# Kernel tuning notes

Measured on AMD Instinct MI355X. Metric: run time of the kernel, lower is better.

Reference implementation:

```python
import jax, jax.numpy as jnp
import numpy as np

N_IN = 2_000_000
N_OUT = 250_000
C_IN = 32
C_OUT = 64
K_VOL = 8  # 2x2x2 kernel, stride 2
EPS = 1e-5


def setup_inputs() -> dict:
    key = jax.random.key(0)
    ks = jax.random.split(key, 6)
    return {
        "in_feats": jax.random.normal(ks[0], (N_IN, C_IN), dtype=jnp.float32),
        "offset_id": jax.random.randint(ks[1], (N_IN,), 0, K_VOL, dtype=jnp.int32),
        "out_idx": jax.random.randint(ks[2], (N_IN,), 0, N_OUT, dtype=jnp.int32),
        "weight": jax.random.normal(ks[3], (K_VOL, C_IN, C_OUT), dtype=jnp.float32) * 0.05,
        "gamma": jnp.ones((3, C_OUT), dtype=jnp.float32),
        "beta": jnp.zeros((3, C_OUT), dtype=jnp.float32),
        "context": jax.random.normal(ks[4], (256,), dtype=jnp.float32),
        "ctx_w": jax.random.normal(ks[5], (256, 2 * C_OUT), dtype=jnp.float32) * 0.02,
        "condition": 1,
    }


def reference(in_feats, offset_id, out_idx, weight, gamma, beta, context, ctx_w, condition):
    # --- sparse conv (stride == kernel): gather-GEMM-scatter per kernel tap ---
    out = jnp.zeros((N_OUT, C_OUT), dtype=in_feats.dtype)
    for k in range(K_VOL):  # fixed small loop over kernel taps
        xk = jnp.where((offset_id == k)[:, None], in_feats, 0.0)  # [N_in, C_in]
        contrib = xk @ weight[k]                                  # [N_in, C_out]
        out = out + jax.ops.segment_sum(contrib, out_idx, num_segments=N_OUT)
    # --- conditional BN (PDNorm-style): per-channel stats, condition-selected affine ---
    mean = jnp.mean(out, axis=0)
    var = jnp.var(out, axis=0)
    normed = (out - mean) * jax.lax.rsqrt(var + EPS)
    normed = normed * gamma[condition] + beta[condition]
    # context modulation: scale/shift from context vector
    scale, shift = jnp.split(context @ ctx_w, 2)  # each [C_out]
    normed = normed * (1.0 + scale) + shift
    # --- ReLU ---
    return jax.nn.relu(normed)
```

## Files before the change

### kernel.cpp

```cpp
#include <hip/hip_runtime.h>

#define N_IN 2000000
#define N_OUT 250000
#define C_IN 32
#define C_OUT 64
#define K_VOL 8
#define EPS 1e-5f
#define CAP 32

#define PT_BLOCKS 7813
#define N_SCAN 250112
#define N_SBLK 977

typedef __attribute__((ext_vector_type(8))) short short8;
typedef __attribute__((ext_vector_type(4))) float f32x4;

#define TA_WHL    250368
#define TA_BSUM   266752
#define TA_SMALL  267776
#define TA_CNT    268288
#define TA_IDXG   1018400
#define TA_POS    (TA_IDXG + N_IN)
#define TA_NEED_BYTES ((size_t)(TA_POS + N_IN) * 4)

#define T1_WT     250000
#define T1_SMALL  266384
#define T1_RLIST  266768
#define T1_NEED_BYTES ((size_t)(T1_RLIST + N_OUT * CAP) * 4)

__global__ __launch_bounds__(256) void k_rank(const int* __restrict__ out_idx,
                                              int* __restrict__ cnt,
                                              int* __restrict__ pos0,
                                              float* __restrict__ smalls) {
    int b = blockIdx.x;
    if (b < PT_BLOCKS) {
        int i = b * 256 + threadIdx.x;
        if (i < N_IN) pos0[i] = atomicAdd(&cnt[out_idx[i]], 1);
    } else {
        if (threadIdx.x < 128) smalls[threadIdx.x] = 0.f;
    }
}

__global__ __launch_bounds__(256) void k_scan_a(const int* __restrict__ cnt,
                                                int* __restrict__ S,
                                                int* __restrict__ bsum) {
    __shared__ int sh[256];
    int t = threadIdx.x;
    int g = blockIdx.x * 256 + t;
    int v = cnt[g];
    sh[t] = v;
    __syncthreads();
#pragma unroll
    for (int off = 1; off < 256; off <<= 1) {
        int a = (t >= off) ? sh[t - off] : 0;
        __syncthreads();
        sh[t] += a;
        __syncthreads();
    }
    S[g] = sh[t] - v;
    if (t == 255) bsum[blockIdx.x] = sh[255];
}

__global__ __launch_bounds__(256) void k_scan_c2(int* __restrict__ S,
                                                 const int* __restrict__ bsum) {
    __shared__ int red[256];
    int t = threadIdx.x, bid = blockIdx.x;
    int acc = 0;
    for (int j = t; j < bid; j += 256) acc += bsum[j];
    red[t] = acc;
    __syncthreads();
#pragma unroll
    for (int off = 128; off > 0; off >>= 1) {
        if (t < off) red[t] += red[t + off];
        __syncthreads();
    }
    S[bid * 256 + t] += red[0];
}

__global__ __launch_bounds__(256) void k_scatidx(const int* __restrict__ out_idx,
                                                 const int* __restrict__ offs,
                                                 const int* __restrict__ pos0,
                                                 const int* __restrict__ S,
                                                 const float* __restrict__ w,
                                                 int* __restrict__ idxg,
                                                 ushort* __restrict__ whl) {
    int b = blockIdx.x;
    if (b < PT_BLOCKS) {
        int i = b * 256 + threadIdx.x;
        if (i >= N_IN) return;
        int o = out_idx[i];
        int tag = offs[i] | ((o & 31) << 3);
        idxg[S[o] + pos0[i]] = i | (tag << 21);
    } else {
        int e = (b - PT_BLOCKS) * 256 + threadIdx.x;
        int c = e >> 11, t = (e >> 9) & 3, l = (e >> 3) & 63, kp = e & 7;
        int j = 4 * c + (l >> 4);
        int n = t * 16 + (l & 15);
        float v = w[kp * 2048 + j * 64 + n];
        unsigned bits = __float_as_uint(v);
        float lo = v - __uint_as_float(bits & 0xFFFF0000u);
        whl[e]         = (ushort)(bits >> 16);
        whl[16384 + e] = (ushort)(__float_as_uint(lo) >> 16);
    }
}

__global__ __launch_bounds__(256) void k_gconv12(const float* __restrict__ xf,
                                                 const int* __restrict__ idxg,
                                                 const int* __restrict__ Sarr,
                                                 const ushort* __restrict__ whl,
                                                 float* __restrict__ out) {
    __shared__ float vxl[4 * 3104];
    int lane = threadIdx.x & 63;
    int wv = threadIdx.x >> 6;
    int g = blockIdx.x * 4 + wv;
    int base = g * 8;
    if (base >= N_OUT) return;
    float* VX = vxl + wv * 3104;
    short* XT = (short*)VX;

    int s = Sarr[base];
    int e = Sarr[base + 8];
    int slot = lane >> 3, jq = lane & 7;

    int tgt4[4];
#pragma unroll
    for (int m = 0; m < 4; ++m) {
        int bin0 = m * 16 + (lane & 15);
        tgt4[m] = (((base + (bin0 >> 3)) & 31) << 3) | (bin0 & 7);
    }

    f32x4 acc1[4][2];
#pragma unroll
    for (int m = 0; m < 4; ++m)
#pragma unroll
        for (int n = 0; n < 2; ++n)
            acc1[m][n] = (f32x4){0.f, 0.f, 0.f, 0.f};

    auto LOADBLK = [&](int p0, float4* xvv, int* tvv) {
        int pk[4];
#pragma unroll
        for (int q = 0; q < 4; ++q) {
            int p = p0 + q * 8 + slot;
            int pc = p < e ? p : e - 1;
            pk[q] = idxg[pc];
        }
#pragma unroll
        for (int q = 0; q < 4; ++q) {
            int p = p0 + q * 8 + slot;
            int idx = pk[q] & 0x1FFFFF;
            tvv[q] = (pk[q] >> 21) & 0xFF;
            xvv[q] = *(const float4*)(xf + (size_t)idx * 32 + jq * 4);
            if (p >= e) xvv[q] = make_float4(0.f, 0.f, 0.f, 0.f);
        }
    };
    auto STAGE = [&](int bb, const float4* xvv, const int* tvv) {
        short* Xh = XT + bb * 3104;
        short* Xl = Xh + 1536;
        unsigned char* TGb = (unsigned char*)(Xh + 3072);
#pragma unroll
        for (int q = 0; q < 4; ++q) {
            int wpos = ((q ^ (jq & 3)) << 3) + slot;
#pragma unroll
            for (int i = 0; i < 4; ++i) {
                float v = (i == 0) ? xvv[q].x : (i == 1) ? xvv[q].y
                         : (i == 2) ? xvv[q].z : xvv[q].w;
                unsigned b = __float_as_uint(v);
                float lo = v - __uint_as_float(b & 0xFFFF0000u);
                int ch = 4 * jq + i;
                Xh[ch * 48 + wpos] = (short)(b >> 16);
                Xl[ch * 48 + wpos] = (short)(__float_as_uint(lo) >> 16);
            }
            if (jq == 0) TGb[q * 8 + slot] = (unsigned char)tvv[q];
        }
    };

    if (e > s) {
        float4 xvA[4], xvB[4], xvC[4];
        int tvA[4], tvB[4], tvC[4];
        int nIt = (e - s + 31) >> 5;
        LOADBLK(s, xvA, tvA);
        LOADBLK(s + 32, xvB, tvB);
        STAGE(0, xvA, tvA);
        for (int it = 0; it < nIt; ++it) {
            int cur = it & 1;
            if (it + 2 < nIt) LOADBLK(s + (it + 2) * 32, xvC, tvC);

            asm volatile("s_waitcnt lgkmcnt(0)" ::: "memory");

            const short* Xh = XT + cur * 3104;
            const short* Xl = Xh + 1536;
            const unsigned char* TGb = (const unsigned char*)(Xh + 3072);
            unsigned long long t8 = *(const unsigned long long*)(TGb + 8 * (lane >> 4));
            int tgv[8];
#pragma unroll
            for (int e2 = 0; e2 < 8; ++e2) tgv[e2] = (int)((t8 >> (8 * e2)) & 0xFF);
            short8 bhf[2], blf[2];
#pragma unroll
            for (int n = 0; n < 2; ++n) {
                int ch = n * 16 + (lane & 15);
                int off = ch * 48 + 8 * ((lane >> 4) ^ ((ch >> 2) & 3));
                bhf[n] = *(const short8*)(Xh + off);
                blf[n] = *(const short8*)(Xl + off);
            }

            if (it + 1 < nIt) STAGE(cur ^ 1, xvB, tvB);
            __builtin_amdgcn_sched_barrier(0);

#pragma unroll
            for (int m = 0; m < 4; ++m) {
                short8 ah;
#pragma unroll
                for (int e2 = 0; e2 < 8; ++e2)
                    ah[e2] = (tgv[e2] == tgt4[m]) ? (short)0x3F80 : (short)0;
#pragma unroll
                for (int n = 0; n < 2; ++n) {
                    acc1[m][n] = __builtin_amdgcn_mfma_f32_16x16x32_bf16(ah, bhf[n], acc1[m][n], 0, 0, 0);
                    acc1[m][n] = __builtin_amdgcn_mfma_f32_16x16x32_bf16(ah, blf[n], acc1[m][n], 0, 0, 0);
                }
            }

            if (it + 1 < nIt) {
#pragma unroll
                for (int q = 0; q < 4; ++q) { xvB[q] = xvC[q]; tvB[q] = tvC[q]; }
            }
        }
    }

    asm volatile("s_waitcnt lgkmcnt(0)" ::: "memory");

#pragma unroll
    for (int m = 0; m < 4; ++m)
#pragma unroll
        for (int n = 0; n < 2; ++n)
#pragma unroll
            for (int reg = 0; reg < 4; ++reg) {
                int bin = m * 16 + (lane >> 4) * 4 + reg;
                VX[(bin >> 3) * 289 + (n * 16 + (lane & 15)) * 9 + (bin & 7)] = acc1[m][n][reg];
            }

    __builtin_amdgcn_sched_barrier(0);
    asm volatile("s_waitcnt lgkmcnt(0)" ::: "memory");
    __builtin_amdgcn_sched_barrier(0);

    int o = lane >> 4;
    int n16 = lane & 15;
    f32x4 zacc = {0.f, 0.f, 0.f, 0.f};
    f32x4 acc0 = zacc, accA = zacc, accB = zacc, accC = zacc;
    const short8* wh = (const short8*)whl;
    const short8* wl = wh + 2048;

#pragma unroll
    for (int c = 0; c < 8; ++c) {
        float a[8];
        if (n16 < 8) {
            const float* src = VX + n16 * 289 + (4 * c + o) * 9;
#pragma unroll
            for (int el = 0; el < 8; ++el) a[el] = src[el];
        } else {
#pragma unroll
            for (int el = 0; el < 8; ++el) a[el] = 0.f;
        }
        short8 ahi, alo;
#pragma unroll
        for (int el = 0; el < 8; ++el) {
            unsigned b = __float_as_uint(a[el]);
            ahi[el] = (short)(b >> 16);
            float lo = a[el] - __uint_as_float(b & 0xFFFF0000u);
            alo[el] = (short)(__float_as_uint(lo) >> 16);
        }
#pragma unroll
        for (int t = 0; t < 4; ++t) {
            short8 bh = wh[(c * 4 + t) * 64 + lane];
            short8 bl = wl[(c * 4 + t) * 64 + lane];
            f32x4* pa = (t == 0) ? &acc0 : (t == 1) ? &accA : (t == 2) ? &accB : &accC;
            *pa = __builtin_amdgcn_mfma_f32_16x16x32_bf16(ahi, bh, *pa, 0, 0, 0);
            *pa = __builtin_amdgcn_mfma_f32_16x16x32_bf16(alo, bh, *pa, 0, 0, 0);
            *pa = __builtin_amdgcn_mfma_f32_16x16x32_bf16(ahi, bl, *pa, 0, 0, 0);
        }
    }

    if (o < 2) {
#pragma unroll
        for (int t = 0; t < 4; ++t) {
            f32x4 a = (t == 0) ? acc0 : (t == 1) ? accA : (t == 2) ? accB : accC;
#pragma unroll
            for (int reg = 0; reg < 4; ++reg)
                out[(size_t)(base + o * 4 + reg) * 64 + t * 16 + n16] = a[reg];
        }
    }
}


__global__ __launch_bounds__(256) void k_stats(const float* __restrict__ out,
                                               float* __restrict__ sums,
                                               float* __restrict__ sumsq) {
    int t = threadIdx.x;
    long stride = (long)gridDim.x * 256;
    float s = 0.f, q = 0.f;
    for (long i = (long)blockIdx.x * 256 + t; i < (long)N_OUT * C_OUT; i += stride) {
        float v = out[i];
        s += v;
        q = fmaf(v, v, q);
    }
    __shared__ float ls[256], lq[256];
    ls[t] = s; lq[t] = q;
    __syncthreads();
    if (t < 64) {
        s = ls[t] + ls[t + 64] + ls[t + 128] + ls[t + 192];
        q = lq[t] + lq[t + 64] + lq[t + 128] + lq[t + 192];
        atomicAdd(&sums[t], s);
        atomicAdd(&sumsq[t], q);
    }
}

__global__ __launch_bounds__(256) void k_ctxprep(const float* __restrict__ context,
                                                 const float* __restrict__ ctx_w,
                                                 const float* __restrict__ sums,
                                                 const float* __restrict__ sumsq,
                                                 const float* __restrict__ gamma,
                                                 const float* __restrict__ beta,
                                                 const int* __restrict__ cond,
                                                 float* __restrict__ AB) {
    __shared__ float part[256];
    __shared__ float ctxv[128];
    int t = threadIdx.x;
    int col = t & 127, half = t >> 7;
    float s = 0.f;
    for (int r = half * 128; r < half * 128 + 128; ++r)
        s = fmaf(context[r], ctx_w[r * 128 + col], s);
    part[t] = s;
    __syncthreads();
    if (t < 128) ctxv[t] = part[t] + part[t + 128];
    __syncthreads();
    if (t < 64) {
        float mean = sums[t] * (1.f / N_OUT);
        float var  = sumsq[t] * (1.f / N_OUT) - mean * mean;
        float inv  = rsqrtf(var + EPS);
        int cd = cond[0];
        float gm = gamma[cd * C_OUT + t], bt = beta[cd * C_OUT + t];
        float sc = 1.f + ctxv[t];
        float sh = ctxv[64 + t];
        AB[t]      = inv * gm * sc;
        AB[64 + t] = (bt - mean * inv * gm) * sc + sh;
    }
}

__global__ __launch_bounds__(256) void k_norm(float* __restrict__ out,
                                              const float* __restrict__ AB) {
    __shared__ float4 lA[16], lB[16];
    int t = threadIdx.x;
    if (t < 16) {
        lA[t] = ((const float4*)AB)[t];
        lB[t] = ((const float4*)AB)[16 + t];
    }
    __syncthreads();
    const long total4 = (long)N_OUT * C_OUT / 4;
    long stride = (long)gridDim.x * 256;
    for (long i = (long)blockIdx.x * 256 + t; i < total4; i += stride) {
        float4 v = ((float4*)out)[i];
        float4 a = lA[i & 15], b = lB[i & 15];
        v.x = fmaxf(fmaf(v.x, a.x, b.x), 0.f);
        v.y = fmaxf(fmaf(v.y, a.y, b.y), 0.f);
        v.z = fmaxf(fmaf(v.z, a.z, b.z), 0.f);
        v.w = fmaxf(fmaf(v.w, a.w, b.w), 0.f);
        ((float4*)out)[i] = v;
    }
}


__global__ __launch_bounds__(256) void k_scat2(const int* __restrict__ out_idx,
                                               const int* __restrict__ offs,
                                               const float* __restrict__ w,
                                               int* __restrict__ cnt,
                                               int* __restrict__ rlist,
                                               ushort* __restrict__ whl) {
    int b = blockIdx.x;
    if (b < PT_BLOCKS) {
        int i = b * 256 + threadIdx.x;
        if (i < N_IN) {
            int o = out_idx[i];
            int pos = atomicAdd(&cnt[o], 1);
            if (pos < CAP) rlist[o * CAP + pos] = i | (offs[i] << 21);
        }
    } else {
        int e = (b - PT_BLOCKS) * 256 + threadIdx.x;
        int c = e >> 11, t = (e >> 9) & 3, l = (e >> 3) & 63, kp = e & 7;
        int j = 4 * c + (l >> 4);
        int n = t * 16 + (l & 15);
        float v = w[kp * 2048 + j * 64 + n];
        unsigned bits = __float_as_uint(v);
        float lo = v - __uint_as_float(bits & 0xFFFF0000u);
        whl[e]         = (ushort)(bits >> 16);
        whl[16384 + e] = (ushort)(__float_as_uint(lo) >> 16);
    }
}

__global__ __launch_bounds__(128) void k_gconv3(const float* __restrict__ xf,
                                                const int* __restrict__ cnt,
                                                const int* __restrict__ rlist,
                                                const ushort* __restrict__ whl,
                                                float* __restrict__ out) {
    __shared__ float vxl[2 * 4640];
    int lane = threadIdx.x & 63;
    int wv = threadIdx.x >> 6;
    int g = blockIdx.x * 2 + wv;
    int base = g * 16;
    if (base >= N_OUT) return;
    float* VX = vxl + wv * 4640;

    float4* z4 = (float4*)VX;
    float4 zz = make_float4(0.f, 0.f, 0.f, 0.f);
#pragma unroll
    for (int i = 0; i < 19; ++i) {
        int p = i * 64 + lane;
        if (p < 1156) z4[p] = zz;
    }

    int slot = lane >> 3, jq = lane & 7;
    int cv = cnt[base + (lane & 15)];
    const int* rbase = rlist + (size_t)base * CAP;
    int pkA = rbase[slot * CAP + jq];
    int pkB = rbase[(8 + slot) * CAP + jq];
    int pkC = rbase[slot * CAP + 8 + jq];
    int pkD = rbase[(8 + slot) * CAP + 8 + jq];

#pragma unroll
    for (int r = 0; r < 16; ++r) {
        int cr = __builtin_amdgcn_readlane(cv, r);
        if (cr > CAP) cr = CAP;
        if (cr == 0) continue;
        {
            int pk = __shfl(r < 8 ? pkA : pkB, (r & 7) * 8 + slot, 64);
            int idx = pk & 0x1FFFFF; if (idx > N_IN - 1) idx = N_IN - 1;
            int kp = (pk >> 21) & 7;
            const float4 x = *(const float4*)(xf + (size_t)idx * 32 + jq * 4);
            float* dst = VX + r * 289 + 36 * jq + kp;
            if (slot < cr) {
                atomicAdd(dst + 0,  x.x);
                atomicAdd(dst + 9,  x.y);
                atomicAdd(dst + 18, x.z);
                atomicAdd(dst + 27, x.w);
            }
        }
        if (cr > 8) {
            int pk = __shfl(r < 8 ? pkC : pkD, (r & 7) * 8 + slot, 64);
            int idx = pk & 0x1FFFFF; if (idx > N_IN - 1) idx = N_IN - 1;
            int kp = (pk >> 21) & 7;
            const float4 x = *(const float4*)(xf + (size_t)idx * 32 + jq * 4);
            float* dst = VX + r * 289 + 36 * jq + kp;
            if (8 + slot < cr) {
                atomicAdd(dst + 0,  x.x);
                atomicAdd(dst + 9,  x.y);
                atomicAdd(dst + 18, x.z);
                atomicAdd(dst + 27, x.w);
            }
        }
        if (cr > 16) {
            for (int p0 = 16; p0 < cr; p0 += 8) {
                int pp = p0 + slot; if (pp > cr - 1) pp = cr - 1;
                int pk = rlist[((size_t)base + r) * CAP + pp];
                int idx = pk & 0x1FFFFF; if (idx > N_IN - 1) idx = N_IN - 1;
                int kp = (pk >> 21) & 7;
                const float4 x = *(const float4*)(xf + (size_t)idx * 32 + jq * 4);
                float* dst = VX + r * 289 + 36 * jq + kp;
                if (p0 + slot < cr) {
                    atomicAdd(dst + 0,  x.x);
                    atomicAdd(dst + 9,  x.y);
                    atomicAdd(dst + 18, x.z);
                    atomicAdd(dst + 27, x.w);
                }
            }
        }
    }

    __builtin_amdgcn_sched_barrier(0);
    asm volatile("s_waitcnt lgkmcnt(0)" ::: "memory");
    __builtin_amdgcn_sched_barrier(0);

    int o = lane >> 4;
    int n16 = lane & 15;
    f32x4 zacc = {0.f, 0.f, 0.f, 0.f};
    f32x4 acc0 = zacc, acc1 = zacc, acc2 = zacc, acc3 = zacc;
    const short8* wh = (const short8*)whl;
    const short8* wl = wh + 2048;

#pragma unroll
    for (int c = 0; c < 8; ++c) {
        const float* src = VX + n16 * 289 + (4 * c + o) * 9;
        float a[8];
#pragma unroll
        for (int el = 0; el < 8; ++el) a[el] = src[el];
        short8 ahi, alo;
#pragma unroll
        for (int el = 0; el < 8; ++el) {
            unsigned b = __float_as_uint(a[el]);
            ahi[el] = (short)(b >> 16);
            float lo = a[el] - __uint_as_float(b & 0xFFFF0000u);
            alo[el] = (short)(__float_as_uint(lo) >> 16);
        }
#pragma unroll
        for (int t = 0; t < 4; ++t) {
            short8 bh = wh[(c * 4 + t) * 64 + lane];
            short8 bl = wl[(c * 4 + t) * 64 + lane];
            f32x4* pa = (t == 0) ? &acc0 : (t == 1) ? &acc1 : (t == 2) ? &acc2 : &acc3;
            *pa = __builtin_amdgcn_mfma_f32_16x16x32_bf16(ahi, bh, *pa, 0, 0, 0);
            *pa = __builtin_amdgcn_mfma_f32_16x16x32_bf16(alo, bh, *pa, 0, 0, 0);
            *pa = __builtin_amdgcn_mfma_f32_16x16x32_bf16(ahi, bl, *pa, 0, 0, 0);
        }
    }

#pragma unroll
    for (int t = 0; t < 4; ++t) {
        f32x4 a = (t == 0) ? acc0 : (t == 1) ? acc1 : (t == 2) ? acc2 : acc3;
#pragma unroll
        for (int reg = 0; reg < 4; ++reg)
            out[(size_t)(base + o * 4 + reg) * 64 + t * 16 + n16] = a[reg];
    }
}


extern "C" void kernel_launch(void* const* d_in, const int* in_sizes, int n_in,
                              void* d_out, int out_size, void* d_ws, size_t ws_size,
                              hipStream_t stream) {
    const float* in_feats = (const float*)d_in[0];
    const int*   offs     = (const int*)d_in[1];
    const int*   out_idx  = (const int*)d_in[2];
    const float* weight   = (const float*)d_in[3];
    const float* gamma    = (const float*)d_in[4];
    const float* beta     = (const float*)d_in[5];
    const float* context  = (const float*)d_in[6];
    const float* ctx_w    = (const float*)d_in[7];
    const int*   cond     = (const int*)d_in[8];
    float* out = (float*)d_out;

    int*   wsi = (int*)d_ws;
    float* wsf = (float*)d_ws;

    if (ws_size >= TA_NEED_BYTES) {
        int*    S      = wsi;
        ushort* whl    = (ushort*)(wsf + TA_WHL);
        int*    bsum   = wsi + TA_BSUM;
        float*  smalls = wsf + TA_SMALL;
        int*    cnt    = wsi + TA_CNT;
        int*    idxg   = wsi + TA_IDXG;
        int*    pos0   = wsi + TA_POS;

        hipMemsetAsync(cnt, 0, (size_t)N_SCAN * 4, stream);

        k_rank<<<PT_BLOCKS + 1, 256, 0, stream>>>(out_idx, cnt, pos0, smalls);
        k_scan_a<<<N_SBLK, 256, 0, stream>>>(cnt, S, bsum);
        k_scan_c2<<<N_SBLK, 256, 0, stream>>>(S, bsum);
        k_scatidx<<<PT_BLOCKS + 64, 256, 0, stream>>>(out_idx, offs, pos0, S,
                                                      weight, idxg, whl);
        k_gconv12<<<7813, 256, 0, stream>>>(in_feats, idxg, wsi, whl, out);

        k_stats<<<2048, 256, 0, stream>>>(out, smalls, smalls + 64);
        k_ctxprep<<<1, 256, 0, stream>>>(context, ctx_w, smalls, smalls + 64,
                                         gamma, beta, cond, smalls + 128);
        k_norm<<<2048, 256, 0, stream>>>(out, smalls + 128);
    } else {
        int*    cnt    = wsi;
        ushort* whl    = (ushort*)(wsf + T1_WT);
        float*  smalls = wsf + T1_SMALL;
        int*    rlist  = wsi + T1_RLIST;

        hipMemsetAsync(cnt, 0, (size_t)N_OUT * 4, stream);
        hipMemsetAsync(smalls, 0, 128 * 4, stream);

        k_scat2<<<PT_BLOCKS + 64, 256, 0, stream>>>(out_idx, offs, weight, cnt, rlist, whl);
        k_gconv3<<<7813, 128, 0, stream>>>(in_feats, cnt, rlist, whl, out);

        k_stats<<<2048, 256, 0, stream>>>(out, smalls, smalls + 64);
        k_ctxprep<<<1, 256, 0, stream>>>(context, ctx_w, smalls, smalls + 64,
                                         gamma, beta, cond, smalls + 128);
        k_norm<<<2048, 256, 0, stream>>>(out, smalls + 128);
    }
}
```

Before: 408.2 us.

## Fuse BN statistics into the gather-conv epilogue with per-wave partials

The conv kernel now reduces per-channel sum and sum-of-squares from its MFMA accumulators. Each wave writes its partials to a channel-major workspace buffer, and a small 128-block kernel reduces them. This replaces the separate k_stats pass that re-read the full 64 MB output. The cost is extra shuffles and stores in the conv epilogue, a larger workspace, and reliance on rows outside the valid range contributing zero to the partials.

```diff
diff --git a/kernel.cpp b/kernel.cpp
--- a/kernel.cpp
+++ b/kernel.cpp
@@ -11,6 +11,7 @@
 #define PT_BLOCKS 7813
 #define N_SCAN 250112
 #define N_SBLK 977
+#define NWAVE 31252
 
 typedef __attribute__((ext_vector_type(8))) short short8;
 typedef __attribute__((ext_vector_type(4))) float f32x4;
@@ -21,24 +22,20 @@
 #define TA_CNT    268288
 #define TA_IDXG   1018400
 #define TA_POS    (TA_IDXG + N_IN)
-#define TA_NEED_BYTES ((size_t)(TA_POS + N_IN) * 4)
+#define TA_PART   (TA_POS + N_IN)
+#define TA_NEED_BYTES ((size_t)(TA_PART + 128 * NWAVE) * 4)
 
 #define T1_WT     250000
 #define T1_SMALL  266384
 #define T1_RLIST  266768
 #define T1_NEED_BYTES ((size_t)(T1_RLIST + N_OUT * CAP) * 4)
 
+
 __global__ __launch_bounds__(256) void k_rank(const int* __restrict__ out_idx,
                                               int* __restrict__ cnt,
-                                              int* __restrict__ pos0,
-                                              float* __restrict__ smalls) {
-    int b = blockIdx.x;
-    if (b < PT_BLOCKS) {
-        int i = b * 256 + threadIdx.x;
-        if (i < N_IN) pos0[i] = atomicAdd(&cnt[out_idx[i]], 1);
-    } else {
-        if (threadIdx.x < 128) smalls[threadIdx.x] = 0.f;
-    }
+                                              int* __restrict__ pos0) {
+    int i = blockIdx.x * 256 + threadIdx.x;
+    if (i < N_IN) pos0[i] = atomicAdd(&cnt[out_idx[i]], 1);
 }
 
 __global__ __launch_bounds__(256) void k_scan_a(const int* __restrict__ cnt,
@@ -104,11 +101,12 @@
     }
 }
 
-__global__ __launch_bounds__(256) void k_gconv12(const float* __restrict__ xf,
+__global__ __launch_bounds__(256) void k_gconv14(const float* __restrict__ xf,
                                                  const int* __restrict__ idxg,
                                                  const int* __restrict__ Sarr,
                                                  const ushort* __restrict__ whl,
-                                                 float* __restrict__ out) {
+                                                 float* __restrict__ out,
+                                                 float* __restrict__ part) {
     __shared__ float vxl[4 * 3104];
     int lane = threadIdx.x & 63;
     int wv = threadIdx.x >> 6;
@@ -288,6 +286,52 @@
                 out[(size_t)(base + o * 4 + reg) * 64 + t * 16 + n16] = a[reg];
         }
     }
+
+    float sv[4], qv[4];
+#pragma unroll
+    for (int t = 0; t < 4; ++t) {
+        f32x4 a = (t == 0) ? acc0 : (t == 1) ? accA : (t == 2) ? accB : accC;
+        float sa = 0.f, qa = 0.f;
+#pragma unroll
+        for (int reg = 0; reg < 4; ++reg) {
+            sa += a[reg];
+            qa = fmaf(a[reg], a[reg], qa);
+        }
+        sv[t] = sa; qv[t] = qa;
+    }
+#pragma unroll
+    for (int t = 0; t < 4; ++t) {
+        sv[t] += __shfl_xor(sv[t], 16, 64);
+        sv[t] += __shfl_xor(sv[t], 32, 64);
+        qv[t] += __shfl_xor(qv[t], 16, 64);
+        qv[t] += __shfl_xor(qv[t], 32, 64);
+    }
+    if (lane < 16) {
+#pragma unroll
+        for (int t = 0; t < 4; ++t) {
+            int ch = t * 16 + lane;
+            part[(size_t)ch * NWAVE + g]        = sv[t];
+            part[(size_t)(64 + ch) * NWAVE + g] = qv[t];
+        }
+    }
+}
+
+__global__ __launch_bounds__(256) void k_statsred(const float* __restrict__ part,
+                                                  float* __restrict__ smalls) {
+    __shared__ float red[256];
+    int c = blockIdx.x;
+    int t = threadIdx.x;
+    const float* p = part + (size_t)c * NWAVE;
+    float s = 0.f;
+    for (int g = t; g < 31250; g += 256) s += p[g];
+    red[t] = s;
+    __syncthreads();
+#pragma unroll
+    for (int off = 128; off > 0; off >>= 1) {
+        if (t < off) red[t] += red[t + off];
+        __syncthreads();
+    }
+    if (t == 0) smalls[c] = red[0];
 }
 
 
@@ -544,17 +588,18 @@
         int*    cnt    = wsi + TA_CNT;
         int*    idxg   = wsi + TA_IDXG;
         int*    pos0   = wsi + TA_POS;
+        float*  part   = wsf + TA_PART;
 
         hipMemsetAsync(cnt, 0, (size_t)N_SCAN * 4, stream);
 
-        k_rank<<<PT_BLOCKS + 1, 256, 0, stream>>>(out_idx, cnt, pos0, smalls);
+        k_rank<<<PT_BLOCKS, 256, 0, stream>>>(out_idx, cnt, pos0);
         k_scan_a<<<N_SBLK, 256, 0, stream>>>(cnt, S, bsum);
         k_scan_c2<<<N_SBLK, 256, 0, stream>>>(S, bsum);
         k_scatidx<<<PT_BLOCKS + 64, 256, 0, stream>>>(out_idx, offs, pos0, S,
                                                       weight, idxg, whl);
-        k_gconv12<<<7813, 256, 0, stream>>>(in_feats, idxg, wsi, whl, out);
-
-        k_stats<<<2048, 256, 0, stream>>>(out, smalls, smalls + 64);
+        k_gconv14<<<7813, 256, 0, stream>>>(in_feats, idxg, wsi, whl, out, part);
+
+        k_statsred<<<128, 256, 0, stream>>>(part, smalls);
         k_ctxprep<<<1, 256, 0, stream>>>(context, ctx_w, smalls, smalls + 64,
                                          gamma, beta, cond, smalls + 128);
         k_norm<<<2048, 256, 0, stream>>>(out, smalls + 128);
```

After: 405.5 us. About the same (-0.7%).
